# Kernel tuning notes

Hardware: AMD Instinct MI355X
Metric: run time of the kernel (lower is better)

The kernel has to match this reference:

```python
import jax, jax.numpy as jnp
import numpy as np

DIM = 512
HEADS = 16
KS = 5  # side_dwconv


def setup_inputs() -> dict:
    key = jax.random.key(0)
    ks = jax.random.split(key, 6)
    B, H, W = 8, 32, 32
    x = jax.random.normal(ks[0], (B, H, W, DIM), dtype=jnp.float32)
    # qkv linear (no bias): torch Linear weight [3C, C]
    w_qkv = jax.random.normal(ks[1], (3 * DIM, DIM), dtype=jnp.float32) * (1.0 / np.sqrt(DIM))
    # output projection
    w_proj = jax.random.normal(ks[2], (DIM, DIM), dtype=jnp.float32) * (1.0 / np.sqrt(DIM))
    b_proj = jax.random.normal(ks[3], (DIM,), dtype=jnp.float32) * 0.01
    # depthwise conv kernel: torch Conv2d(groups=dim) weight [C, 1, k, k]
    w_lepe = jax.random.normal(ks[4], (DIM, 1, KS, KS), dtype=jnp.float32) * (1.0 / KS)
    b_lepe = jax.random.normal(ks[5], (DIM,), dtype=jnp.float32) * 0.01
    return {"x": x, "w_qkv": w_qkv, "w_proj": w_proj, "b_proj": b_proj,
            "w_lepe": w_lepe, "b_lepe": b_lepe}


def _depthwise_conv(x_nchw, w, b):
    # x: [B, C, H, W], w: [C, 1, k, k] (OIHW with feature_group_count=C)
    out = jax.lax.conv_general_dilated(
        x_nchw, w,
        window_strides=(1, 1),
        padding=[(KS // 2, KS // 2), (KS // 2, KS // 2)],
        dimension_numbers=("NCHW", "OIHW", "NCHW"),
        feature_group_count=x_nchw.shape[1],
    )
    return out + b[None, :, None, None]


def reference(x, w_qkv, w_proj, b_proj, w_lepe, b_lepe):
    B, H, W, C = x.shape
    N = H * W
    hd = C // HEADS
    scale = hd ** (-0.5)

    xt = x.reshape(B, N, C)  # n (h w) c

    qkv = xt @ w_qkv.T  # [B, N, 3C]
    qkv = qkv.reshape(B, N, 3, HEADS, hd).transpose(2, 0, 3, 1, 4)  # [3, B, h, N, d]
    q, k, v = qkv[0], qkv[1], qkv[2]

    # LePE depthwise conv positional encoding
    lepe = _depthwise_conv(xt.reshape(B, H, W, C).transpose(0, 3, 1, 2), w_lepe, b_lepe)
    lepe = lepe.transpose(0, 2, 3, 1).reshape(B, N, C)

    attn = jnp.einsum("bhnd,bhmd->bhnm", q, k) * scale
    attn = jax.nn.softmax(attn, axis=-1)
    out = jnp.einsum("bhnm,bhmd->bhnd", attn, v)
    out = out.transpose(0, 2, 1, 3).reshape(B, N, C)

    out = out + lepe
    out = out @ w_proj.T + b_proj
    return out.reshape(B, H, W, C)
```

## Files before the change

kernel.cpp:

```cpp
#include <hip/hip_runtime.h>

typedef unsigned int u32;
typedef unsigned short u16;
typedef __attribute__((ext_vector_type(8))) short bfrag;
typedef __attribute__((ext_vector_type(4))) float ffrag;

__device__ __forceinline__ float bf_lo(u32 w) { u32 v = w << 16; return __builtin_bit_cast(float, v); }
__device__ __forceinline__ float bf_hi(u32 w) { u32 v = w & 0xFFFF0000u; return __builtin_bit_cast(float, v); }
__device__ __forceinline__ float bf2f(u16 h) { u32 v = ((u32)h) << 16; return __builtin_bit_cast(float, v); }
__device__ __forceinline__ u16 f2bf_bits(float f) {
  u32 x = __builtin_bit_cast(u32, f);
  x += 0x7FFFu + ((x >> 16) & 1u);
  return (u16)(x >> 16);
}
__device__ __forceinline__ u32 pack2(float a, float b) {
  return (u32)f2bf_bits(a) | ((u32)f2bf_bits(b) << 16);
}
__device__ __forceinline__ u32 bfadd2(u32 a, u32 b) {
  return pack2(bf_lo(a) + bf_lo(b), bf_hi(a) + bf_hi(b));
}

__global__ __launch_bounds__(256) void qkv_gemm(const float* __restrict__ X,
                                                const float* __restrict__ W,
                                                u16* __restrict__ qb,
                                                u16* __restrict__ kb,
                                                u16* __restrict__ vb) {
  __shared__ u16 As[128][40];
  __shared__ u16 Bs[128][40];
  const int tid = threadIdx.x;
  const int lane = tid & 63;
  const int w = tid >> 6;
  const int wr = w >> 1, wc = w & 1;
  const int lrow = lane & 15, quad = lane >> 4;
  const int bm0 = blockIdx.x * 128;
  const int bn0 = blockIdx.y * 128;
  const int lr = tid >> 1;
  const int lc = (tid & 1) * 16;

  ffrag acc[4][4];
#pragma unroll
  for (int i = 0; i < 4; i++)
#pragma unroll
    for (int j = 0; j < 4; j++) acc[i][j] = (ffrag){0.f, 0.f, 0.f, 0.f};

  for (int k0 = 0; k0 < 512; k0 += 32) {
    const float4* ap = (const float4*)(X + (bm0 + lr) * 512 + k0 + lc);
    const float4* bp = (const float4*)(W + (bn0 + lr) * 512 + k0 + lc);
    float4 a0 = ap[0], a1 = ap[1], a2 = ap[2], a3 = ap[3];
    float4 b0 = bp[0], b1 = bp[1], b2 = bp[2], b3 = bp[3];
    __syncthreads();
    u32* as = (u32*)(&As[lr][lc]);
    u32* bs = (u32*)(&Bs[lr][lc]);
    as[0] = pack2(a0.x, a0.y); as[1] = pack2(a0.z, a0.w);
    as[2] = pack2(a1.x, a1.y); as[3] = pack2(a1.z, a1.w);
    as[4] = pack2(a2.x, a2.y); as[5] = pack2(a2.z, a2.w);
    as[6] = pack2(a3.x, a3.y); as[7] = pack2(a3.z, a3.w);
    bs[0] = pack2(b0.x, b0.y); bs[1] = pack2(b0.z, b0.w);
    bs[2] = pack2(b1.x, b1.y); bs[3] = pack2(b1.z, b1.w);
    bs[4] = pack2(b2.x, b2.y); bs[5] = pack2(b2.z, b2.w);
    bs[6] = pack2(b3.x, b3.y); bs[7] = pack2(b3.z, b3.w);
    __syncthreads();
    bfrag af[4], bf[4];
#pragma unroll
    for (int i = 0; i < 4; i++) af[i] = *(const bfrag*)(&As[wr * 64 + i * 16 + lrow][quad * 8]);
#pragma unroll
    for (int j = 0; j < 4; j++) bf[j] = *(const bfrag*)(&Bs[wc * 64 + j * 16 + lrow][quad * 8]);
#pragma unroll
    for (int i = 0; i < 4; i++)
#pragma unroll
      for (int j = 0; j < 4; j++)
        acc[i][j] = __builtin_amdgcn_mfma_f32_16x16x32_bf16(af[i], bf[j], acc[i][j], 0, 0, 0);
  }

#pragma unroll
  for (int i = 0; i < 4; i++)
#pragma unroll
    for (int j = 0; j < 4; j++) {
      int jj = bn0 + wc * 64 + j * 16 + lrow;
      int which = jj >> 9, rem = jj & 511;
      int h = rem >> 5, d = rem & 31;
      u16* dst = (which == 0) ? qb : (which == 1) ? kb : vb;
#pragma unroll
      for (int r = 0; r < 4; r++) {
        int m = bm0 + wr * 64 + i * 16 + quad * 4 + r;
        int pair = ((m >> 10) << 4) + h;
        int n = m & 1023;
        dst[(pair * 1024 + n) * 32 + d] = f2bf_bits(acc[i][j][r]);
      }
    }
}

__global__ __launch_bounds__(256) void lepe_conv(const float* __restrict__ X,
                                                 const float* __restrict__ Wl,
                                                 const float* __restrict__ bl,
                                                 u16* __restrict__ out) {
  __shared__ float Wls[512 * 25];
  const int tid = threadIdx.x;
  const int c = tid * 2;
  const int y = blockIdx.x;
  const int b = blockIdx.y;
  const int x0 = blockIdx.z * 16;

  {
    const float2* src = (const float2*)Wl;
    float2* dst = (float2*)Wls;
#pragma unroll
    for (int i = 0; i < 25; i++) dst[tid + i * 256] = src[tid + i * 256];
  }
  __syncthreads();

  float w0[25], w1[25];
#pragma unroll
  for (int t = 0; t < 25; t++) {
    w0[t] = Wls[c * 25 + t];
    w1[t] = Wls[(c + 1) * 25 + t];
  }
  const float2 bias = *(const float2*)(bl + c);

  const float* rowp[5];
  bool rowv[5];
#pragma unroll
  for (int r = 0; r < 5; r++) {
    int yy = y + r - 2;
    rowv[r] = (yy >= 0) && (yy < 32);
    rowp[r] = X + ((b * 32 + (rowv[r] ? yy : 0)) * 32) * 512 + c;
  }

  float2 win[5][5];
#pragma unroll
  for (int rel = -2; rel <= 1; rel++) {
    const int slot = ((rel % 5) + 5) % 5;
    const int xcol = x0 + rel;
    const bool xv = (xcol >= 0) && (xcol < 32);
#pragma unroll
    for (int r = 0; r < 5; r++)
      win[r][slot] = (xv && rowv[r]) ? *(const float2*)(rowp[r] + xcol * 512)
                                     : float2{0.f, 0.f};
  }

#pragma unroll
  for (int xi = 0; xi < 16; xi++) {
    {
      const int slot = (xi + 2) % 5;
      const int xcol = x0 + xi + 2;
      const bool xv = (xcol < 32);
#pragma unroll
      for (int r = 0; r < 5; r++)
        win[r][slot] = (xv && rowv[r]) ? *(const float2*)(rowp[r] + xcol * 512)
                                       : float2{0.f, 0.f};
    }
    float a0 = bias.x, a1 = bias.y;
#pragma unroll
    for (int ky = 0; ky < 5; ky++)
#pragma unroll
      for (int kx = 0; kx < 5; kx++) {
        const int rel = xi - 2 + kx;
        const int slot = ((rel % 5) + 5) % 5;
        const float2 v = win[ky][slot];
        const int t = ky * 5 + kx;
        a0 = fmaf(v.x, w0[t], a0);
        a1 = fmaf(v.y, w1[t], a1);
      }
    const int sp = (b * 32 + y) * 32 + x0 + xi;
    *(u32*)(out + sp * 512 + c) = pack2(a0, a1);
  }
}

__global__ __launch_bounds__(256) void attn_mfma(const u16* __restrict__ qb,
                                                 const u16* __restrict__ kb,
                                                 const u16* __restrict__ vb,
                                                 u16* __restrict__ ao) {
  __shared__ u32 Vt[32][132];
  __shared__ u32 Ps[4][16][20];
  const int tid = threadIdx.x, lane = tid & 63, w = tid >> 6;
  const int quad = lane >> 4, m16 = lane & 15;
  const int pair = blockIdx.x >> 2;
  const int quarter = blockIdx.x & 3;
  const int b = pair >> 4, h = pair & 15;

  const int wq0 = quarter * 256 + w * 64;
  bfrag qf[4];
#pragma unroll
  for (int i = 0; i < 4; i++) {
    int row = wq0 + i * 16 + m16;
    qf[i] = *(const bfrag*)(qb + (pair * 1024 + row) * 32 + quad * 8);
  }

  const float SC = 0.17677669529663687f;
  const u16* kbase = kb + pair * 32768;
  const u16* vbase = vb + pair * 32768;
  float lrow[16];
  ffrag oacc[4][2];
#pragma unroll
  for (int s = 0; s < 16; s++) lrow[s] = 0.f;
#pragma unroll
  for (int i = 0; i < 4; i++) {
    oacc[i][0] = (ffrag){0.f, 0.f, 0.f, 0.f};
    oacc[i][1] = (ffrag){0.f, 0.f, 0.f, 0.f};
  }

  for (int jc = 0; jc < 1024; jc += 256) {
    __syncthreads();
#pragma unroll
    for (int it = 0; it < 2; it++) {
      int task = tid + it * 256;
      int pp = task & 127;
      int q = task >> 7;
      int g = pp >> 4, t = pp & 15;
      int jlo = jc + g * 32 + t;
      uint4 vl = *(const uint4*)(vbase + jlo * 32 + q * 8);
      uint4 vh = *(const uint4*)(vbase + (jlo + 16) * 32 + q * 8);
      u32 lw[4] = {vl.x, vl.y, vl.z, vl.w};
      u32 hw[4] = {vh.x, vh.y, vh.z, vh.w};
#pragma unroll
      for (int e = 0; e < 4; e++) {
        int d0 = q * 8 + e * 2;
        Vt[d0][pp]     = (lw[e] & 0xFFFFu) | (hw[e] << 16);
        Vt[d0 + 1][pp] = (lw[e] >> 16) | (hw[e] & 0xFFFF0000u);
      }
    }
    __syncthreads();

    for (int j0 = 0; j0 < 256; j0 += 32) {
      const int jk = jc + j0;
      const int g0 = j0 >> 5;
      bfrag kf0 = *(const bfrag*)(kbase + (jk + m16) * 32 + quad * 8);
      bfrag kf1 = *(const bfrag*)(kbase + (jk + 16 + m16) * 32 + quad * 8);
      ffrag s[4][2];
#pragma unroll
      for (int i = 0; i < 4; i++) {
        s[i][0] = __builtin_amdgcn_mfma_f32_16x16x32_bf16(qf[i], kf0, (ffrag){0.f,0.f,0.f,0.f}, 0, 0, 0);
        s[i][1] = __builtin_amdgcn_mfma_f32_16x16x32_bf16(qf[i], kf1, (ffrag){0.f,0.f,0.f,0.f}, 0, 0, 0);
      }
      bfrag vf0 = *(const bfrag*)(&Vt[m16][g0 * 16 + quad * 4]);
      bfrag vf1 = *(const bfrag*)(&Vt[16 + m16][g0 * 16 + quad * 4]);

#pragma unroll
      for (int i = 0; i < 4; i++) {
#pragma unroll
        for (int r = 0; r < 4; r++) {
          float p0 = __expf(fmaf(s[i][0][r], SC, -8.0f));
          float p1 = __expf(fmaf(s[i][1][r], SC, -8.0f));
          lrow[i * 4 + r] += p0 + p1;
          Ps[w][quad * 4 + r][m16] =
              (__builtin_bit_cast(u32, p0) >> 16) | (__builtin_bit_cast(u32, p1) & 0xFFFF0000u);
        }
        bfrag pf = *(const bfrag*)(&Ps[w][m16][quad * 4]);
        oacc[i][0] = __builtin_amdgcn_mfma_f32_16x16x32_bf16(pf, vf0, oacc[i][0], 0, 0, 0);
        oacc[i][1] = __builtin_amdgcn_mfma_f32_16x16x32_bf16(pf, vf1, oacc[i][1], 0, 0, 0);
      }
    }
  }

  float linv[16];
#pragma unroll
  for (int s = 0; s < 16; s++) {
    float l = lrow[s];
    l += __shfl_xor(l, 1);
    l += __shfl_xor(l, 2);
    l += __shfl_xor(l, 4);
    l += __shfl_xor(l, 8);
    linv[s] = 1.0f / l;
  }
#pragma unroll
  for (int i = 0; i < 4; i++)
#pragma unroll
    for (int jd = 0; jd < 2; jd++)
#pragma unroll
      for (int r = 0; r < 4; r++) {
        int row = wq0 + i * 16 + quad * 4 + r;
        int col = jd * 16 + m16;
        ao[(b * 1024 + row) * 512 + h * 32 + col] = f2bf_bits(oacc[i][jd][r] * linv[i * 4 + r]);
      }
}

__global__ __launch_bounds__(256) void proj_gemm(const u16* __restrict__ Y1,
                                                 const u16* __restrict__ Y2,
                                                 const float* __restrict__ W,
                                                 const float* __restrict__ bp,
                                                 float* __restrict__ out) {
  __shared__ u16 As[128][40];
  __shared__ u16 Bs[128][40];
  const int tid = threadIdx.x;
  const int lane = tid & 63;
  const int w = tid >> 6;
  const int wr = w >> 1, wc = w & 1;
  const int lrow = lane & 15, quad = lane >> 4;
  const int bm0 = blockIdx.x * 128;
  const int bn0 = blockIdx.y * 128;
  const int lr = tid >> 1;
  const int lc = (tid & 1) * 16;

  ffrag acc[4][4];
#pragma unroll
  for (int i = 0; i < 4; i++)
#pragma unroll
    for (int j = 0; j < 4; j++) acc[i][j] = (ffrag){0.f, 0.f, 0.f, 0.f};

  for (int k0 = 0; k0 < 512; k0 += 32) {
    const u16* y1p = Y1 + (bm0 + lr) * 512 + k0 + lc;
    const u16* y2p = Y2 + (bm0 + lr) * 512 + k0 + lc;
    uint4 a10 = *(const uint4*)(y1p);
    uint4 a11 = *(const uint4*)(y1p + 8);
    uint4 a20 = *(const uint4*)(y2p);
    uint4 a21 = *(const uint4*)(y2p + 8);
    const float4* wp = (const float4*)(W + (bn0 + lr) * 512 + k0 + lc);
    float4 b0 = wp[0], b1 = wp[1], b2 = wp[2], b3 = wp[3];
    uint4 av0, av1;
    av0.x = bfadd2(a10.x, a20.x); av0.y = bfadd2(a10.y, a20.y);
    av0.z = bfadd2(a10.z, a20.z); av0.w = bfadd2(a10.w, a20.w);
    av1.x = bfadd2(a11.x, a21.x); av1.y = bfadd2(a11.y, a21.y);
    av1.z = bfadd2(a11.z, a21.z); av1.w = bfadd2(a11.w, a21.w);
    __syncthreads();
    *(uint4*)(&As[lr][lc])     = av0;
    *(uint4*)(&As[lr][lc + 8]) = av1;
    u32* bs = (u32*)(&Bs[lr][lc]);
    bs[0] = pack2(b0.x, b0.y); bs[1] = pack2(b0.z, b0.w);
    bs[2] = pack2(b1.x, b1.y); bs[3] = pack2(b1.z, b1.w);
    bs[4] = pack2(b2.x, b2.y); bs[5] = pack2(b2.z, b2.w);
    bs[6] = pack2(b3.x, b3.y); bs[7] = pack2(b3.z, b3.w);
    __syncthreads();
    bfrag af[4], bf[4];
#pragma unroll
    for (int i = 0; i < 4; i++) af[i] = *(const bfrag*)(&As[wr * 64 + i * 16 + lrow][quad * 8]);
#pragma unroll
    for (int j = 0; j < 4; j++) bf[j] = *(const bfrag*)(&Bs[wc * 64 + j * 16 + lrow][quad * 8]);
#pragma unroll
    for (int i = 0; i < 4; i++)
#pragma unroll
      for (int j = 0; j < 4; j++)
        acc[i][j] = __builtin_amdgcn_mfma_f32_16x16x32_bf16(af[i], bf[j], acc[i][j], 0, 0, 0);
  }

#pragma unroll
  for (int i = 0; i < 4; i++)
#pragma unroll
    for (int j = 0; j < 4; j++) {
      int jj = bn0 + wc * 64 + j * 16 + lrow;
      float bias = bp[jj];
#pragma unroll
      for (int r = 0; r < 4; r++) {
        int m = bm0 + wr * 64 + i * 16 + quad * 4 + r;
        out[m * 512 + jj] = acc[i][j][r] + bias;
      }
    }
}

extern "C" void kernel_launch(void* const* d_in, const int* in_sizes, int n_in,
                              void* d_out, int out_size, void* d_ws, size_t ws_size,
                              hipStream_t stream) {
  const float* x      = (const float*)d_in[0];
  const float* w_qkv  = (const float*)d_in[1];
  const float* w_proj = (const float*)d_in[2];
  const float* b_proj = (const float*)d_in[3];
  const float* w_lepe = (const float*)d_in[4];
  const float* b_lepe = (const float*)d_in[5];
  float* out = (float*)d_out;

  char* ws = (char*)d_ws;
  const size_t SEG = 8388608;
  u16* qb = (u16*)(ws + 0 * SEG);
  u16* kb = (u16*)(ws + 1 * SEG);
  u16* vb = (u16*)(ws + 2 * SEG);
  u16* ao = (u16*)(ws + 3 * SEG);
  u16* lp = (u16*)(ws + 4 * SEG);

  hipLaunchKernelGGL(qkv_gemm, dim3(64, 12), dim3(256), 0, stream, x, w_qkv, qb, kb, vb);
  hipLaunchKernelGGL(lepe_conv, dim3(32, 8, 2), dim3(256), 0, stream, x, w_lepe, b_lepe, lp);
  hipLaunchKernelGGL(attn_mfma, dim3(512), dim3(256), 0, stream, qb, kb, vb, ao);
  hipLaunchKernelGGL(proj_gemm, dim3(64, 4), dim3(256), 0, stream, ao, lp, w_proj, b_proj, out);
}
```

Measured before the change: 193.8 us.

## Use 8-wave attention blocks with exp2 softmax, MFMA row sums and K prefetch

The attention kernel now runs 512-thread blocks, and each wave owns 32 query rows instead of 64. This halves per-wave register state and doubles the waves available for latency hiding, with launch bounds set for higher residency. The exponent is now a direct exp2 builtin with the scale and shift folded into log2 units. The per-row softmax denominators come from an extra MFMA against a ones fragment, which replaces the scalar accumulation and the shuffle reductions. K fragments for the next 32-key step are prefetched into registers. The prefetch reads one block past the end of each head's K on the last iteration, which stays inside the workspace. The extra MFMA per row tile adds matrix-unit work.

```diff
diff --git a/kernel.cpp b/kernel.cpp
--- a/kernel.cpp
+++ b/kernel.cpp
@@ -18,6 +18,13 @@
 }
 __device__ __forceinline__ u32 bfadd2(u32 a, u32 b) {
   return pack2(bf_lo(a) + bf_lo(b), bf_hi(a) + bf_hi(b));
+}
+__device__ __forceinline__ float fast_exp2(float x) {
+#if __has_builtin(__builtin_amdgcn_exp2f)
+  return __builtin_amdgcn_exp2f(x);
+#else
+  return __expf(x * 0.6931471805599453f);
+#endif
 }
 
 __global__ __launch_bounds__(256) void qkv_gemm(const float* __restrict__ X,
@@ -166,44 +173,50 @@
   }
 }
 
-__global__ __launch_bounds__(256) void attn_mfma(const u16* __restrict__ qb,
-                                                 const u16* __restrict__ kb,
-                                                 const u16* __restrict__ vb,
-                                                 u16* __restrict__ ao) {
+__global__ __launch_bounds__(512, 4) void attn_mfma(const u16* __restrict__ qb,
+                                                    const u16* __restrict__ kb,
+                                                    const u16* __restrict__ vb,
+                                                    u16* __restrict__ ao) {
   __shared__ u32 Vt[32][132];
-  __shared__ u32 Ps[4][16][20];
+  __shared__ u32 Ps[8][16][20];
   const int tid = threadIdx.x, lane = tid & 63, w = tid >> 6;
   const int quad = lane >> 4, m16 = lane & 15;
   const int pair = blockIdx.x >> 2;
   const int quarter = blockIdx.x & 3;
   const int b = pair >> 4, h = pair & 15;
 
-  const int wq0 = quarter * 256 + w * 64;
-  bfrag qf[4];
-#pragma unroll
-  for (int i = 0; i < 4; i++) {
+  const int wq0 = quarter * 256 + w * 32;
+  bfrag qf[2];
+#pragma unroll
+  for (int i = 0; i < 2; i++) {
     int row = wq0 + i * 16 + m16;
     qf[i] = *(const bfrag*)(qb + (pair * 1024 + row) * 32 + quad * 8);
   }
 
-  const float SC = 0.17677669529663687f;
+  const float SC2 = 0.25503448540239605f;
+  const float SHIFT2 = 11.541560327111707f;
   const u16* kbase = kb + pair * 32768;
   const u16* vbase = vb + pair * 32768;
-  float lrow[16];
-  ffrag oacc[4][2];
-#pragma unroll
-  for (int s = 0; s < 16; s++) lrow[s] = 0.f;
-#pragma unroll
-  for (int i = 0; i < 4; i++) {
+
+  bfrag onesf;
+#pragma unroll
+  for (int e = 0; e < 8; e++) onesf[e] = (short)0x3F80;
+
+  ffrag oacc[2][2], sacc[2];
+#pragma unroll
+  for (int i = 0; i < 2; i++) {
     oacc[i][0] = (ffrag){0.f, 0.f, 0.f, 0.f};
     oacc[i][1] = (ffrag){0.f, 0.f, 0.f, 0.f};
-  }
+    sacc[i]    = (ffrag){0.f, 0.f, 0.f, 0.f};
+  }
+
+  bfrag kf0n = *(const bfrag*)(kbase + (m16) * 32 + quad * 8);
+  bfrag kf1n = *(const bfrag*)(kbase + (16 + m16) * 32 + quad * 8);
 
   for (int jc = 0; jc < 1024; jc += 256) {
     __syncthreads();
-#pragma unroll
-    for (int it = 0; it < 2; it++) {
-      int task = tid + it * 256;
+    {
+      int task = tid;
       int pp = task & 127;
       int q = task >> 7;
       int g = pp >> 4, t = pp & 15;
@@ -222,13 +235,16 @@
     __syncthreads();
 
     for (int j0 = 0; j0 < 256; j0 += 32) {
-      const int jk = jc + j0;
       const int g0 = j0 >> 5;
-      bfrag kf0 = *(const bfrag*)(kbase + (jk + m16) * 32 + quad * 8);
-      bfrag kf1 = *(const bfrag*)(kbase + (jk + 16 + m16) * 32 + quad * 8);
-      ffrag s[4][2];
-#pragma unroll
-      for (int i = 0; i < 4; i++) {
+      bfrag kf0 = kf0n, kf1 = kf1n;
+      {
+        const int jn = jc + j0 + 32;
+        kf0n = *(const bfrag*)(kbase + (jn + m16) * 32 + quad * 8);
+        kf1n = *(const bfrag*)(kbase + (jn + 16 + m16) * 32 + quad * 8);
+      }
+      ffrag s[2][2];
+#pragma unroll
+      for (int i = 0; i < 2; i++) {
         s[i][0] = __builtin_amdgcn_mfma_f32_16x16x32_bf16(qf[i], kf0, (ffrag){0.f,0.f,0.f,0.f}, 0, 0, 0);
         s[i][1] = __builtin_amdgcn_mfma_f32_16x16x32_bf16(qf[i], kf1, (ffrag){0.f,0.f,0.f,0.f}, 0, 0, 0);
       }
@@ -236,42 +252,36 @@
       bfrag vf1 = *(const bfrag*)(&Vt[16 + m16][g0 * 16 + quad * 4]);
 
 #pragma unroll
-      for (int i = 0; i < 4; i++) {
+      for (int i = 0; i < 2; i++) {
 #pragma unroll
         for (int r = 0; r < 4; r++) {
-          float p0 = __expf(fmaf(s[i][0][r], SC, -8.0f));
-          float p1 = __expf(fmaf(s[i][1][r], SC, -8.0f));
-          lrow[i * 4 + r] += p0 + p1;
+          float p0 = fast_exp2(fmaf(s[i][0][r], SC2, -SHIFT2));
+          float p1 = fast_exp2(fmaf(s[i][1][r], SC2, -SHIFT2));
           Ps[w][quad * 4 + r][m16] =
               (__builtin_bit_cast(u32, p0) >> 16) | (__builtin_bit_cast(u32, p1) & 0xFFFF0000u);
         }
         bfrag pf = *(const bfrag*)(&Ps[w][m16][quad * 4]);
         oacc[i][0] = __builtin_amdgcn_mfma_f32_16x16x32_bf16(pf, vf0, oacc[i][0], 0, 0, 0);
         oacc[i][1] = __builtin_amdgcn_mfma_f32_16x16x32_bf16(pf, vf1, oacc[i][1], 0, 0, 0);
-      }
-    }
-  }
-
-  float linv[16];
-#pragma unroll
-  for (int s = 0; s < 16; s++) {
-    float l = lrow[s];
-    l += __shfl_xor(l, 1);
-    l += __shfl_xor(l, 2);
-    l += __shfl_xor(l, 4);
-    l += __shfl_xor(l, 8);
-    linv[s] = 1.0f / l;
-  }
-#pragma unroll
-  for (int i = 0; i < 4; i++)
+        sacc[i]    = __builtin_amdgcn_mfma_f32_16x16x32_bf16(pf, onesf, sacc[i], 0, 0, 0);
+      }
+    }
+  }
+
+#pragma unroll
+  for (int i = 0; i < 2; i++) {
+    float inv[4];
+#pragma unroll
+    for (int r = 0; r < 4; r++) inv[r] = 1.0f / sacc[i][r];
 #pragma unroll
     for (int jd = 0; jd < 2; jd++)
 #pragma unroll
       for (int r = 0; r < 4; r++) {
         int row = wq0 + i * 16 + quad * 4 + r;
         int col = jd * 16 + m16;
-        ao[(b * 1024 + row) * 512 + h * 32 + col] = f2bf_bits(oacc[i][jd][r] * linv[i * 4 + r]);
-      }
+        ao[(b * 1024 + row) * 512 + h * 32 + col] = f2bf_bits(oacc[i][jd][r] * inv[r]);
+      }
+  }
 }
 
 __global__ __launch_bounds__(256) void proj_gemm(const u16* __restrict__ Y1,
@@ -367,6 +377,6 @@
 
   hipLaunchKernelGGL(qkv_gemm, dim3(64, 12), dim3(256), 0, stream, x, w_qkv, qb, kb, vb);
   hipLaunchKernelGGL(lepe_conv, dim3(32, 8, 2), dim3(256), 0, stream, x, w_lepe, b_lepe, lp);
-  hipLaunchKernelGGL(attn_mfma, dim3(512), dim3(256), 0, stream, qb, kb, vb, ao);
+  hipLaunchKernelGGL(attn_mfma, dim3(512), dim3(512), 0, stream, qb, kb, vb, ao);
   hipLaunchKernelGGL(proj_gemm, dim3(64, 4), dim3(256), 0, stream, ao, lp, w_proj, b_proj, out);
 }
```

Result: faster. 181.5 us (-6.4%).
